# Performance work log

Hardware: AMD Instinct MI355X
Metric: run time of the kernel (lower is better)

Reference implementation:

```python
import jax, jax.numpy as jnp
import numpy as np

N_HEAD = 16

def setup_inputs() -> dict:
    key = jax.random.key(0)
    k1, k2, k3 = jax.random.split(key, 3)
    B, T, C = 4, 2048, 2048
    x = jax.random.normal(k1, (B, T, C), dtype=jnp.float32)
    # nn.Linear weights stored as [out, in]; we keep [in, out] for x @ W
    Wqkv = jax.random.normal(k2, (C, 3 * C), dtype=jnp.float32) * (1.0 / np.sqrt(C))
    Wproj = jax.random.normal(k3, (C, C), dtype=jnp.float32) * (1.0 / np.sqrt(C))
    return {"x": x, "Wqkv": Wqkv, "Wproj": Wproj}

def reference(x, Wqkv, Wproj):
    B, T, C = x.shape
    H = N_HEAD
    hd = C // H
    qkv = x @ Wqkv                                  # [B,T,3C]
    qkv = qkv.reshape(B, T, 3, H, hd)
    q = qkv[:, :, 0].transpose(0, 2, 1, 3)          # [B,H,T,hd]
    k = qkv[:, :, 1].transpose(0, 2, 1, 3)
    v = qkv[:, :, 2].transpose(0, 2, 1, 3)
    scale = 1.0 / np.sqrt(hd).astype(np.float32)
    scores = jnp.einsum('bhqd,bhkd->bhqk', q, k) * scale
    causal = jnp.tril(jnp.ones((T, T), dtype=bool))
    scores = jnp.where(causal, scores, jnp.finfo(scores.dtype).min)
    attn = jax.nn.softmax(scores, axis=-1)
    y = jnp.einsum('bhqk,bhkd->bhqd', attn, v)      # [B,H,T,hd]
    y = y.transpose(0, 2, 1, 3).reshape(B, T, C)
    return y @ Wproj  # dropout is identity in eval / p=0
```

## Files before the change

### kernel.cpp

```cpp
#include <hip/hip_runtime.h>
#include <hip/hip_bf16.h>
#include <cstdint>

typedef __bf16 bf16;
typedef __bf16 bf16x8 __attribute__((ext_vector_type(8)));
typedef float f32x4 __attribute__((ext_vector_type(4)));
typedef float f32x8 __attribute__((ext_vector_type(8)));
typedef uint32_t u32x4 __attribute__((ext_vector_type(4)));

constexpr int Bz = 4, T = 2048, Cdim = 2048, NH = 16, HD = 128;
constexpr int QKVC = 3 * Cdim;
constexpr int QKC = 2 * Cdim;
constexpr float NEG_BIG = -3.0e4f;

__device__ __forceinline__ void load_lds16(const bf16* g, const bf16* l) {
  __builtin_amdgcn_global_load_lds(
      (const __attribute__((address_space(1))) void*)g,
      (__attribute__((address_space(3))) void*)l, 16, 0, 0);
}

__device__ __forceinline__ uint32_t pack2bf(float lo, float hi) {
  uint16_t a = __builtin_bit_cast(uint16_t, (bf16)lo);
  uint16_t b = __builtin_bit_cast(uint16_t, (bf16)hi);
  return ((uint32_t)b << 16) | (uint32_t)a;
}

__global__ __launch_bounds__(256)
void cvt_bf16_k(const float* __restrict__ in, bf16* __restrict__ out) {
  size_t i = (size_t)blockIdx.x * 256 + threadIdx.x;
  f32x8 v = *(const f32x8*)(in + i * 8);
  bf16x8 h;
#pragma unroll
  for (int j = 0; j < 8; ++j) h[j] = (bf16)v[j];
  *(bf16x8*)(out + i * 8) = h;
}

__global__ __launch_bounds__(256)
void transpose_cvt_k(const float* __restrict__ in, bf16* __restrict__ out,
                     int R, int Ccols) {
  __shared__ bf16 tile[32][33];
  int c0 = blockIdx.x * 32, r0 = blockIdx.y * 32;
  int tx = threadIdx.x, ty = threadIdx.y;
#pragma unroll
  for (int i = 0; i < 4; ++i)
    tile[ty + i * 8][tx] = (bf16)in[(size_t)(r0 + ty + i * 8) * Ccols + c0 + tx];
  __syncthreads();
#pragma unroll
  for (int i = 0; i < 4; ++i)
    out[(size_t)(c0 + ty + i * 8) * R + r0 + tx] = tile[tx][ty + i * 8];
}

template <bool CF32, bool SCATV>
__global__ __launch_bounds__(512, 2)
void gemm256_k(const bf16* __restrict__ A, const bf16* __restrict__ BT,
               void* __restrict__ Craw, bf16* __restrict__ Vt,
               int M, int N, int K, int ldc) {
  extern __shared__ bf16 lds[];
  const int nK = K >> 6;

  const int nbx = gridDim.x;
  const int nwg = nbx * gridDim.y;
  const int orig = blockIdx.x + blockIdx.y * nbx;
  const int q8 = nwg >> 3;
  const int wgid = (orig & 7) * q8 + (orig >> 3);
  const size_t col0 = (size_t)(wgid % nbx) * 256;
  const size_t row0 = (size_t)(wgid / nbx) * 256;

  const int tid = threadIdx.x;
  const int w = tid >> 6, lane = tid & 63;
  const int qn = lane & 15, quad = lane >> 4;
  const int wm = w >> 2, wn = w & 3;

  const int rl8 = lane >> 3;
  const int scol = ((lane & 7) ^ rl8) << 3;
  const size_t gOff = (size_t)(w * 8 + rl8) * K + scol;
  const int ldsW = w * 512;

  const int csA0 = (quad * 8) ^ ((qn & 7) << 3);
  const int csA1 = (32 + quad * 8) ^ ((qn & 7) << 3);
  const int aBaseIdx = wm * 8192 + qn * 64;
  const int bBaseIdx = 16384 + (wn >> 1) * 8192 + ((wn & 1) * 64 + qn) * 64;

  f32x4 acc[8][4];
  f32x4 zero4 = {0.f, 0.f, 0.f, 0.f};
#pragma unroll
  for (int m = 0; m < 8; ++m)
#pragma unroll
    for (int n = 0; n < 4; ++n) acc[m][n] = zero4;

  auto stageA = [&](int c, int h, int t) {
    const bf16* g = A + (row0 + h * 128) * (size_t)K + (size_t)t * 64 + gOff;
    const bf16* l = lds + c * 32768 + h * 8192 + ldsW;
    load_lds16(g, l);
    load_lds16(g + (size_t)64 * K, l + 4096);
  };
  auto stageB = [&](int c, int h, int t) {
    const bf16* g = BT + (col0 + h * 128) * (size_t)K + (size_t)t * 64 + gOff;
    const bf16* l = lds + c * 32768 + 16384 + h * 8192 + ldsW;
    load_lds16(g, l);
    load_lds16(g + (size_t)64 * K, l + 4096);
  };

  stageA(0, 0, 0); stageA(0, 1, 0);
  stageB(0, 0, 0); stageB(0, 1, 0);
  if (nK > 1) { stageB(1, 0, 1); stageB(1, 1, 1); }
  asm volatile("s_waitcnt vmcnt(4)" ::: "memory");
  asm volatile("s_barrier" ::: "memory");

  for (int t = 0; t < nK; ++t) {
    const int c = t & 1, cn = c ^ 1;
    const int cE = c * 32768;

    bf16x8 a0[4][2], b0[2][2], b1[2][2];
#pragma unroll
    for (int m = 0; m < 4; ++m) {
      a0[m][0] = *(const bf16x8*)&lds[cE + aBaseIdx + m * 1024 + csA0];
      a0[m][1] = *(const bf16x8*)&lds[cE + aBaseIdx + m * 1024 + csA1];
    }
#pragma unroll
    for (int n = 0; n < 2; ++n) {
      b0[n][0] = *(const bf16x8*)&lds[cE + bBaseIdx + n * 1024 + csA0];
      b0[n][1] = *(const bf16x8*)&lds[cE + bBaseIdx + n * 1024 + csA1];
      b1[n][0] = *(const bf16x8*)&lds[cE + bBaseIdx + (n + 2) * 1024 + csA0];
      b1[n][1] = *(const bf16x8*)&lds[cE + bBaseIdx + (n + 2) * 1024 + csA1];
    }
    if (t + 1 < nK) stageA(cn, 1, t + 1);
    __builtin_amdgcn_s_setprio(1);
#pragma unroll
    for (int m = 0; m < 4; ++m)
#pragma unroll
      for (int n = 0; n < 2; ++n) {
        acc[m][n] = __builtin_amdgcn_mfma_f32_16x16x32_bf16(a0[m][0], b0[n][0], acc[m][n], 0, 0, 0);
        acc[m][n] = __builtin_amdgcn_mfma_f32_16x16x32_bf16(a0[m][1], b0[n][1], acc[m][n], 0, 0, 0);
      }
    __builtin_amdgcn_s_setprio(0);
    asm volatile("s_barrier" ::: "memory");

    if (t + 1 < nK) stageA(cn, 0, t + 1);
    __builtin_amdgcn_s_setprio(1);
#pragma unroll
    for (int m = 0; m < 4; ++m)
#pragma unroll
      for (int n = 0; n < 2; ++n) {
        acc[m][n + 2] = __builtin_amdgcn_mfma_f32_16x16x32_bf16(a0[m][0], b1[n][0], acc[m][n + 2], 0, 0, 0);
        acc[m][n + 2] = __builtin_amdgcn_mfma_f32_16x16x32_bf16(a0[m][1], b1[n][1], acc[m][n + 2], 0, 0, 0);
      }
    __builtin_amdgcn_s_setprio(0);
    asm volatile("s_barrier" ::: "memory");

    bf16x8 a1[4][2];
#pragma unroll
    for (int m = 0; m < 4; ++m) {
      a1[m][0] = *(const bf16x8*)&lds[cE + aBaseIdx + (m + 4) * 1024 + csA0];
      a1[m][1] = *(const bf16x8*)&lds[cE + aBaseIdx + (m + 4) * 1024 + csA1];
    }
    if (t + 2 < nK) stageB(c, 0, t + 2);
    __builtin_amdgcn_s_setprio(1);
#pragma unroll
    for (int m = 0; m < 4; ++m)
#pragma unroll
      for (int n = 0; n < 2; ++n) {
        acc[m + 4][n] = __builtin_amdgcn_mfma_f32_16x16x32_bf16(a1[m][0], b0[n][0], acc[m + 4][n], 0, 0, 0);
        acc[m + 4][n] = __builtin_amdgcn_mfma_f32_16x16x32_bf16(a1[m][1], b0[n][1], acc[m + 4][n], 0, 0, 0);
      }
    __builtin_amdgcn_s_setprio(0);
    asm volatile("s_barrier" ::: "memory");

    if (t + 2 < nK) {
      stageB(c, 1, t + 2);
      asm volatile("s_waitcnt vmcnt(4)" ::: "memory");
    } else {
      asm volatile("s_waitcnt vmcnt(0)" ::: "memory");
    }
    __builtin_amdgcn_s_setprio(1);
#pragma unroll
    for (int m = 0; m < 4; ++m)
#pragma unroll
      for (int n = 0; n < 2; ++n) {
        acc[m + 4][n + 2] = __builtin_amdgcn_mfma_f32_16x16x32_bf16(a1[m][0], b1[n][0], acc[m + 4][n + 2], 0, 0, 0);
        acc[m + 4][n + 2] = __builtin_amdgcn_mfma_f32_16x16x32_bf16(a1[m][1], b1[n][1], acc[m + 4][n + 2], 0, 0, 0);
      }
    __builtin_amdgcn_s_setprio(0);
    asm volatile("s_barrier" ::: "memory");
  }

  if (SCATV && (int)col0 >= QKC) {
#pragma unroll
    for (int m = 0; m < 8; ++m)
#pragma unroll
      for (int n = 0; n < 4; ++n)
#pragma unroll
        for (int rr = 0; rr < 4; ++rr) {
          int row = (int)row0 + wm * 128 + m * 16 + quad * 4 + rr;
          int bb = row >> 11, tt = row & (T - 1);
          int cv = (int)col0 + wn * 64 + n * 16 + qn - QKC;
          int hh = cv >> 7, d = cv & 127;
          Vt[((size_t)(bb * NH + hh) * HD + d) * T + tt] = (bf16)acc[m][n][rr];
        }
  } else {
#pragma unroll
    for (int m = 0; m < 8; ++m)
#pragma unroll
      for (int n = 0; n < 4; ++n)
#pragma unroll
        for (int rr = 0; rr < 4; ++rr) {
          size_t idx = (row0 + wm * 128 + m * 16 + quad * 4 + rr) * (size_t)ldc +
                       col0 + wn * 64 + n * 16 + qn;
          if (CF32) ((float*)Craw)[idx] = acc[m][n][rr];
          else      ((bf16*)Craw)[idx] = (bf16)acc[m][n][rr];
        }
  }
}

constexpr int KSTR = 136, VSTR = 72;

__global__ __launch_bounds__(512, 2)
void attn_k(const bf16* __restrict__ qk, const bf16* __restrict__ vt,
            bf16* __restrict__ y) {
  const int b = blockIdx.z, h = blockIdx.y;
  const int qbA = blockIdx.x;
  const int qbB = 15 - qbA;
  const int tid = threadIdx.x;
  const int w = tid >> 6, lane = tid & 63;
  const int qn = lane & 15, quad = lane >> 4;
  const int q0A = qbA * 128 + w * 16;
  const int q0B = qbB * 128 + w * 16;

  __shared__ __align__(16) bf16 Ks[64 * KSTR];
  __shared__ __align__(16) bf16 Vs[128 * VSTR];

  const bf16* qkB = qk + (size_t)b * T * QKC + h * HD;
  const bf16* vtB = vt + (size_t)(b * NH + h) * HD * T;
  const bf16* kBase = qkB + Cdim;

  bf16x8 qFA[4], qFB[4];
  {
    const float scale = 0.088388347648318447f;
    const bf16* qRowA = qkB + (size_t)(q0A + qn) * QKC;
    const bf16* qRowB = qkB + (size_t)(q0B + qn) * QKC;
#pragma unroll
    for (int c = 0; c < 4; ++c) {
      bf16x8 va = *(const bf16x8*)(qRowA + c * 32 + quad * 8);
      bf16x8 vb = *(const bf16x8*)(qRowB + c * 32 + quad * 8);
#pragma unroll
      for (int j = 0; j < 8; ++j) {
        va[j] = (bf16)((float)va[j] * scale);
        vb[j] = (bf16)((float)vb[j] * scale);
      }
      qFA[c] = va; qFB[c] = vb;
    }
  }

  float mA = NEG_BIG, lA = 0.f, mB = NEG_BIG, lB = 0.f;
  f32x4 zero4 = {0.f, 0.f, 0.f, 0.f};
  f32x4 oA[8], oB[8];
#pragma unroll
  for (int cc = 0; cc < 8; ++cc) { oA[cc] = zero4; oB[cc] = zero4; }

  const int kr  = tid >> 4;
  const int kc8 = (tid & 15) << 3;
  const int vd  = tid >> 3;
  const int vk8 = (tid & 7) << 3;

  const int addrA = ((lane & 15) + ((quad & 1) << 5)) << 2;
  const int addrB = addrA + 64;
  const int hi2 = quad >> 1;

  auto softmax_pack = [&](f32x4 (&s)[4], int q0p, int kt0, float& m_i,
                          float& l_i, f32x4 (&o)[8], uint32_t (&pku)[4][2]) {
    if (kt0 + 63 > q0p) {
      const int qv = q0p + qn;
#pragma unroll
      for (int ks = 0; ks < 4; ++ks)
#pragma unroll
        for (int rr = 0; rr < 4; ++rr)
          if (kt0 + ks * 16 + quad * 4 + rr > qv) s[ks][rr] = NEG_BIG;
    }
    float mx = s[0][0];
#pragma unroll
    for (int ks = 0; ks < 4; ++ks)
#pragma unroll
      for (int rr = 0; rr < 4; ++rr) mx = fmaxf(mx, s[ks][rr]);
    mx = fmaxf(mx, __shfl_xor(mx, 16));
    mx = fmaxf(mx, __shfl_xor(mx, 32));
    if (!__all(mx - m_i <= 8.0f)) {
      float mn = fmaxf(m_i, mx);
      float alpha = __expf(m_i - mn);
      m_i = mn;
      l_i *= alpha;
      float aR[4];
#pragma unroll
      for (int rr = 0; rr < 4; ++rr) aR[rr] = __shfl(alpha, quad * 4 + rr);
#pragma unroll
      for (int cc = 0; cc < 8; ++cc)
#pragma unroll
        for (int rr = 0; rr < 4; ++rr) o[cc][rr] *= aR[rr];
    }
    float rs = 0.f;
#pragma unroll
    for (int ks = 0; ks < 4; ++ks)
#pragma unroll
      for (int rr = 0; rr < 4; ++rr) {
        float pv = __expf(s[ks][rr] - m_i);
        s[ks][rr] = pv;
        rs += pv;
      }
    rs += __shfl_xor(rs, 16);
    rs += __shfl_xor(rs, 32);
    l_i += rs;
#pragma unroll
    for (int ks = 0; ks < 4; ++ks)
#pragma unroll
      for (int b2 = 0; b2 < 2; ++b2)
        pku[ks][b2] = pack2bf(s[ks][2 * b2], s[ks][2 * b2 + 1]);
  };

  auto redist = [&](uint32_t (&pku)[4][2], int c) -> bf16x8 {
    uint32_t lo0A = (uint32_t)__builtin_amdgcn_ds_bpermute(addrA, (int)pku[2 * c][0]);
    uint32_t lo1A = (uint32_t)__builtin_amdgcn_ds_bpermute(addrA, (int)pku[2 * c][1]);
    uint32_t lo0B = (uint32_t)__builtin_amdgcn_ds_bpermute(addrB, (int)pku[2 * c][0]);
    uint32_t lo1B = (uint32_t)__builtin_amdgcn_ds_bpermute(addrB, (int)pku[2 * c][1]);
    uint32_t hi0A = (uint32_t)__builtin_amdgcn_ds_bpermute(addrA, (int)pku[2 * c + 1][0]);
    uint32_t hi1A = (uint32_t)__builtin_amdgcn_ds_bpermute(addrA, (int)pku[2 * c + 1][1]);
    uint32_t hi0B = (uint32_t)__builtin_amdgcn_ds_bpermute(addrB, (int)pku[2 * c + 1][0]);
    uint32_t hi1B = (uint32_t)__builtin_amdgcn_ds_bpermute(addrB, (int)pku[2 * c + 1][1]);
    u32x4 pw;
    pw[0] = hi2 ? hi0A : lo0A;
    pw[1] = hi2 ? hi1A : lo1A;
    pw[2] = hi2 ? hi0B : lo0B;
    pw[3] = hi2 ? hi1B : lo1B;
    return __builtin_bit_cast(bf16x8, pw);
  };

  const int nT = 2 * qbB + 2;

  bf16x8 rK0 = *(const bf16x8*)(kBase + (size_t)kr * QKC + kc8);
  bf16x8 rK1 = *(const bf16x8*)(kBase + (size_t)(kr + 32) * QKC + kc8);
  bf16x8 rV0 = *(const bf16x8*)(vtB + (size_t)vd * T + vk8);
  bf16x8 rV1 = *(const bf16x8*)(vtB + (size_t)(vd + 64) * T + vk8);

  for (int t = 0; t < nT; ++t) {
    const int kt0 = t * 64;
    __syncthreads();
    *(bf16x8*)&Ks[kr * KSTR + kc8] = rK0;
    *(bf16x8*)&Ks[(kr + 32) * KSTR + kc8] = rK1;
    *(bf16x8*)&Vs[vd * VSTR + vk8] = rV0;
    *(bf16x8*)&Vs[(vd + 64) * VSTR + vk8] = rV1;
    __syncthreads();
    if (t + 1 < nT) {
      const int kn = kt0 + 64;
      rK0 = *(const bf16x8*)(kBase + (size_t)(kn + kr) * QKC + kc8);
      rK1 = *(const bf16x8*)(kBase + (size_t)(kn + kr + 32) * QKC + kc8);
      rV0 = *(const bf16x8*)(vtB + (size_t)vd * T + kn + vk8);
      rV1 = *(const bf16x8*)(vtB + (size_t)(vd + 64) * T + kn + vk8);
    }
    const bool actA = (kt0 <= q0A + 15);
    const bool actB = (kt0 <= q0B + 15);
    if (!actB) continue;

    f32x4 sA[4] = {zero4, zero4, zero4, zero4};
    f32x4 sB[4] = {zero4, zero4, zero4, zero4};
    __builtin_amdgcn_s_setprio(1);
    if (actA) {
#pragma unroll
      for (int c = 0; c < 4; ++c)
#pragma unroll
        for (int ks = 0; ks < 4; ++ks) {
          bf16x8 kf = *(const bf16x8*)&Ks[(ks * 16 + qn) * KSTR + c * 32 + quad * 8];
          sA[ks] = __builtin_amdgcn_mfma_f32_16x16x32_bf16(kf, qFA[c], sA[ks], 0, 0, 0);
          sB[ks] = __builtin_amdgcn_mfma_f32_16x16x32_bf16(kf, qFB[c], sB[ks], 0, 0, 0);
        }
    } else {
#pragma unroll
      for (int c = 0; c < 4; ++c)
#pragma unroll
        for (int ks = 0; ks < 4; ++ks) {
          bf16x8 kf = *(const bf16x8*)&Ks[(ks * 16 + qn) * KSTR + c * 32 + quad * 8];
          sB[ks] = __builtin_amdgcn_mfma_f32_16x16x32_bf16(kf, qFB[c], sB[ks], 0, 0, 0);
        }
    }
    __builtin_amdgcn_s_setprio(0);

    uint32_t pkuA[4][2], pkuB[4][2];
    if (actA) softmax_pack(sA, q0A, kt0, mA, lA, oA, pkuA);
    softmax_pack(sB, q0B, kt0, mB, lB, oB, pkuB);

    __builtin_amdgcn_s_setprio(1);
    if (actA) {
#pragma unroll
      for (int c = 0; c < 2; ++c) {
        bf16x8 pFA = redist(pkuA, c);
        bf16x8 pFB = redist(pkuB, c);
#pragma unroll
        for (int cc = 0; cc < 8; ++cc) {
          bf16x8 vf = *(const bf16x8*)&Vs[(cc * 16 + qn) * VSTR + c * 32 + quad * 8];
          oA[cc] = __builtin_amdgcn_mfma_f32_16x16x32_bf16(pFA, vf, oA[cc], 0, 0, 0);
          oB[cc] = __builtin_amdgcn_mfma_f32_16x16x32_bf16(pFB, vf, oB[cc], 0, 0, 0);
        }
      }
    } else {
#pragma unroll
      for (int c = 0; c < 2; ++c) {
        bf16x8 pFB = redist(pkuB, c);
#pragma unroll
        for (int cc = 0; cc < 8; ++cc) {
          bf16x8 vf = *(const bf16x8*)&Vs[(cc * 16 + qn) * VSTR + c * 32 + quad * 8];
          oB[cc] = __builtin_amdgcn_mfma_f32_16x16x32_bf16(pFB, vf, oB[cc], 0, 0, 0);
        }
      }
    }
    __builtin_amdgcn_s_setprio(0);
  }

  bf16* yB = y + (size_t)b * T * Cdim + h * HD;
  {
    float linv[4];
#pragma unroll
    for (int rr = 0; rr < 4; ++rr) {
      float lr = __shfl(lA, quad * 4 + rr);
      linv[rr] = 1.f / fmaxf(lr, 1e-30f);
    }
#pragma unroll
    for (int cc = 0; cc < 8; ++cc)
#pragma unroll
      for (int rr = 0; rr < 4; ++rr)
        yB[(size_t)(q0A + quad * 4 + rr) * Cdim + cc * 16 + qn] =
            (bf16)(oA[cc][rr] * linv[rr]);
  }
  {
    float linv[4];
#pragma unroll
    for (int rr = 0; rr < 4; ++rr) {
      float lr = __shfl(lB, quad * 4 + rr);
      linv[rr] = 1.f / fmaxf(lr, 1e-30f);
    }
#pragma unroll
    for (int cc = 0; cc < 8; ++cc)
#pragma unroll
      for (int rr = 0; rr < 4; ++rr)
        yB[(size_t)(q0B + quad * 4 + rr) * Cdim + cc * 16 + qn] =
            (bf16)(oB[cc][rr] * linv[rr]);
  }
}

extern "C" void kernel_launch(void* const* d_in, const int* in_sizes, int n_in,
                              void* d_out, int out_size, void* d_ws, size_t ws_size,
                              hipStream_t stream) {
  const float* x     = (const float*)d_in[0];
  const float* Wqkv  = (const float*)d_in[1];
  const float* Wproj = (const float*)d_in[2];
  float* out = (float*)d_out;

  char* ws = (char*)d_ws;
  bf16* qkbuf  = (bf16*)(ws);
  bf16* Vt     = (bf16*)(ws + (size_t)64 * 1024 * 1024);
  bf16* WqkvT  = (bf16*)(ws + (size_t)96 * 1024 * 1024);
  bf16* y      = WqkvT;
  bf16* WprojT = (bf16*)(ws + (size_t)128 * 1024 * 1024);
  bf16* xb     = (bf16*)d_out;

  cvt_bf16_k<<<dim3((Bz * T * Cdim) / (256 * 8)), 256, 0, stream>>>(x, xb);
  transpose_cvt_k<<<dim3(QKVC / 32, Cdim / 32), dim3(32, 8), 0, stream>>>(
      Wqkv, WqkvT, Cdim, QKVC);
  transpose_cvt_k<<<dim3(Cdim / 32, Cdim / 32), dim3(32, 8), 0, stream>>>(
      Wproj, WprojT, Cdim, Cdim);

  gemm256_k<false, true><<<dim3(QKVC / 256, (Bz * T) / 256), 512, 131072, stream>>>(
      xb, WqkvT, (void*)qkbuf, Vt, Bz * T, QKVC, Cdim, QKC);

  attn_k<<<dim3(T / 256, NH, Bz), 512, 0, stream>>>(qkbuf, Vt, y);

  gemm256_k<true, false><<<dim3(Cdim / 256, (Bz * T) / 256), 512, 131072, stream>>>(
      y, WprojT, (void*)out, nullptr, Bz * T, Cdim, Cdim, Cdim);
}
```

Baseline: 550.3 us.

## Software-pipeline LDS fragment reads across GEMM phases and reorder MFMA k-loop

Restructures the GEMM main loop so LDS fragment reads for the next k-tile (A0/B0) are issued during the last MFMA phase of the current tile, and B1/A1 are read just before the phases that need them. It also reorders MFMAs to iterate the k-half outermost, so consecutive MFMAs hit independent accumulators. The global-to-LDS stage schedule and waitcnt values are shifted to fit. This aims to hide LDS latency behind MFMA work, at the cost of more live registers and subtler correctness reliance on barrier placement.

```diff
diff --git a/kernel.cpp b/kernel.cpp
--- a/kernel.cpp
+++ b/kernel.cpp
@@ -101,85 +101,101 @@
     load_lds16(g + (size_t)64 * K, l + 4096);
   };
 
+  bf16x8 a0[4][2], a1[4][2], b0[2][2], b1[2][2];
+
+  auto rdA0 = [&](int cE) {
+#pragma unroll
+    for (int m = 0; m < 4; ++m) {
+      a0[m][0] = *(const bf16x8*)&lds[cE + aBaseIdx + m * 1024 + csA0];
+      a0[m][1] = *(const bf16x8*)&lds[cE + aBaseIdx + m * 1024 + csA1];
+    }
+  };
+  auto rdA1 = [&](int cE) {
+#pragma unroll
+    for (int m = 0; m < 4; ++m) {
+      a1[m][0] = *(const bf16x8*)&lds[cE + aBaseIdx + (m + 4) * 1024 + csA0];
+      a1[m][1] = *(const bf16x8*)&lds[cE + aBaseIdx + (m + 4) * 1024 + csA1];
+    }
+  };
+  auto rdB0 = [&](int cE) {
+#pragma unroll
+    for (int n = 0; n < 2; ++n) {
+      b0[n][0] = *(const bf16x8*)&lds[cE + bBaseIdx + n * 1024 + csA0];
+      b0[n][1] = *(const bf16x8*)&lds[cE + bBaseIdx + n * 1024 + csA1];
+    }
+  };
+  auto rdB1 = [&](int cE) {
+#pragma unroll
+    for (int n = 0; n < 2; ++n) {
+      b1[n][0] = *(const bf16x8*)&lds[cE + bBaseIdx + (n + 2) * 1024 + csA0];
+      b1[n][1] = *(const bf16x8*)&lds[cE + bBaseIdx + (n + 2) * 1024 + csA1];
+    }
+  };
+
   stageA(0, 0, 0); stageA(0, 1, 0);
   stageB(0, 0, 0); stageB(0, 1, 0);
   if (nK > 1) { stageB(1, 0, 1); stageB(1, 1, 1); }
   asm volatile("s_waitcnt vmcnt(4)" ::: "memory");
   asm volatile("s_barrier" ::: "memory");
+  rdA0(0); rdB0(0);
 
   for (int t = 0; t < nK; ++t) {
     const int c = t & 1, cn = c ^ 1;
-    const int cE = c * 32768;
-
-    bf16x8 a0[4][2], b0[2][2], b1[2][2];
-#pragma unroll
-    for (int m = 0; m < 4; ++m) {
-      a0[m][0] = *(const bf16x8*)&lds[cE + aBaseIdx + m * 1024 + csA0];
-      a0[m][1] = *(const bf16x8*)&lds[cE + aBaseIdx + m * 1024 + csA1];
-    }
-#pragma unroll
-    for (int n = 0; n < 2; ++n) {
-      b0[n][0] = *(const bf16x8*)&lds[cE + bBaseIdx + n * 1024 + csA0];
-      b0[n][1] = *(const bf16x8*)&lds[cE + bBaseIdx + n * 1024 + csA1];
-      b1[n][0] = *(const bf16x8*)&lds[cE + bBaseIdx + (n + 2) * 1024 + csA0];
-      b1[n][1] = *(const bf16x8*)&lds[cE + bBaseIdx + (n + 2) * 1024 + csA1];
-    }
+    const int cE = c * 32768, cnE = cn * 32768;
+
     if (t + 1 < nK) stageA(cn, 1, t + 1);
-    __builtin_amdgcn_s_setprio(1);
-#pragma unroll
-    for (int m = 0; m < 4; ++m)
-#pragma unroll
-      for (int n = 0; n < 2; ++n) {
-        acc[m][n] = __builtin_amdgcn_mfma_f32_16x16x32_bf16(a0[m][0], b0[n][0], acc[m][n], 0, 0, 0);
-        acc[m][n] = __builtin_amdgcn_mfma_f32_16x16x32_bf16(a0[m][1], b0[n][1], acc[m][n], 0, 0, 0);
-      }
+    rdB1(cE);
+    __builtin_amdgcn_s_setprio(1);
+#pragma unroll
+    for (int kh = 0; kh < 2; ++kh)
+#pragma unroll
+      for (int m = 0; m < 4; ++m)
+#pragma unroll
+        for (int n = 0; n < 2; ++n)
+          acc[m][n] = __builtin_amdgcn_mfma_f32_16x16x32_bf16(a0[m][kh], b0[n][kh], acc[m][n], 0, 0, 0);
     __builtin_amdgcn_s_setprio(0);
     asm volatile("s_barrier" ::: "memory");
 
     if (t + 1 < nK) stageA(cn, 0, t + 1);
-    __builtin_amdgcn_s_setprio(1);
-#pragma unroll
-    for (int m = 0; m < 4; ++m)
-#pragma unroll
-      for (int n = 0; n < 2; ++n) {
-        acc[m][n + 2] = __builtin_amdgcn_mfma_f32_16x16x32_bf16(a0[m][0], b1[n][0], acc[m][n + 2], 0, 0, 0);
-        acc[m][n + 2] = __builtin_amdgcn_mfma_f32_16x16x32_bf16(a0[m][1], b1[n][1], acc[m][n + 2], 0, 0, 0);
-      }
+    rdA1(cE);
+    __builtin_amdgcn_s_setprio(1);
+#pragma unroll
+    for (int kh = 0; kh < 2; ++kh)
+#pragma unroll
+      for (int m = 0; m < 4; ++m)
+#pragma unroll
+        for (int n = 0; n < 2; ++n)
+          acc[m][n + 2] = __builtin_amdgcn_mfma_f32_16x16x32_bf16(a0[m][kh], b1[n][kh], acc[m][n + 2], 0, 0, 0);
     __builtin_amdgcn_s_setprio(0);
     asm volatile("s_barrier" ::: "memory");
 
-    bf16x8 a1[4][2];
-#pragma unroll
-    for (int m = 0; m < 4; ++m) {
-      a1[m][0] = *(const bf16x8*)&lds[cE + aBaseIdx + (m + 4) * 1024 + csA0];
-      a1[m][1] = *(const bf16x8*)&lds[cE + aBaseIdx + (m + 4) * 1024 + csA1];
-    }
-    if (t + 2 < nK) stageB(c, 0, t + 2);
-    __builtin_amdgcn_s_setprio(1);
-#pragma unroll
-    for (int m = 0; m < 4; ++m)
-#pragma unroll
-      for (int n = 0; n < 2; ++n) {
-        acc[m + 4][n] = __builtin_amdgcn_mfma_f32_16x16x32_bf16(a1[m][0], b0[n][0], acc[m + 4][n], 0, 0, 0);
-        acc[m + 4][n] = __builtin_amdgcn_mfma_f32_16x16x32_bf16(a1[m][1], b0[n][1], acc[m + 4][n], 0, 0, 0);
-      }
-    __builtin_amdgcn_s_setprio(0);
-    asm volatile("s_barrier" ::: "memory");
-
     if (t + 2 < nK) {
-      stageB(c, 1, t + 2);
-      asm volatile("s_waitcnt vmcnt(4)" ::: "memory");
+      stageB(c, 0, t + 2);
+      asm volatile("s_waitcnt vmcnt(2)" ::: "memory");
     } else {
       asm volatile("s_waitcnt vmcnt(0)" ::: "memory");
     }
     __builtin_amdgcn_s_setprio(1);
 #pragma unroll
-    for (int m = 0; m < 4; ++m)
-#pragma unroll
-      for (int n = 0; n < 2; ++n) {
-        acc[m + 4][n + 2] = __builtin_amdgcn_mfma_f32_16x16x32_bf16(a1[m][0], b1[n][0], acc[m + 4][n + 2], 0, 0, 0);
-        acc[m + 4][n + 2] = __builtin_amdgcn_mfma_f32_16x16x32_bf16(a1[m][1], b1[n][1], acc[m + 4][n + 2], 0, 0, 0);
-      }
+    for (int kh = 0; kh < 2; ++kh)
+#pragma unroll
+      for (int m = 0; m < 4; ++m)
+#pragma unroll
+        for (int n = 0; n < 2; ++n)
+          acc[m + 4][n] = __builtin_amdgcn_mfma_f32_16x16x32_bf16(a1[m][kh], b0[n][kh], acc[m + 4][n], 0, 0, 0);
+    __builtin_amdgcn_s_setprio(0);
+    asm volatile("s_barrier" ::: "memory");
+
+    if (t + 2 < nK) stageB(c, 1, t + 2);
+    if (t + 1 < nK) { rdA0(cnE); rdB0(cnE); }
+    __builtin_amdgcn_s_setprio(1);
+#pragma unroll
+    for (int kh = 0; kh < 2; ++kh)
+#pragma unroll
+      for (int m = 0; m < 4; ++m)
+#pragma unroll
+        for (int n = 0; n < 2; ++n)
+          acc[m + 4][n + 2] = __builtin_amdgcn_mfma_f32_16x16x32_bf16(a1[m][kh], b1[n][kh], acc[m + 4][n + 2], 0, 0, 0);
     __builtin_amdgcn_s_setprio(0);
     asm volatile("s_barrier" ::: "memory");
   }
```

Measured after the change: 560.6 us. No clear change (+1.9%).
